# Performance work log

Measured on AMD Instinct MI355X. Metric: run time of the kernel, lower is better.

## Reference

```python
import jax, jax.numpy as jnp
import numpy as np

B, C, Hf, T = 8, 2, 257, 2048
D_IN = C * Hf          # 514
DM = 256               # d_model
NL = 4                 # n_layers
N = 32                 # S4D complex state size (d_state=64 -> N=32 complex modes)


def setup_inputs() -> dict:
    key = jax.random.key(0)
    ks = jax.random.split(key, 16)
    sc_in = 1.0 / np.sqrt(D_IN)
    sc_dm = 1.0 / np.sqrt(DM)
    inp = {}
    inp['x'] = jax.random.normal(ks[0], (B, C, Hf, T, 2), dtype=jnp.float32)
    # complex encoder (d_input -> d_model)
    inp['enc_Wr'] = jax.random.normal(ks[1], (DM, D_IN), dtype=jnp.float32) * sc_in
    inp['enc_Wi'] = jax.random.normal(ks[2], (DM, D_IN), dtype=jnp.float32) * sc_in
    inp['enc_br'] = jnp.zeros((DM,), jnp.float32)
    inp['enc_bi'] = jnp.zeros((DM,), jnp.float32)
    # per-layer S4D kernel params (stacked over layers)
    lo, hi = np.log(0.001), np.log(0.1)
    inp['log_dt'] = jax.random.uniform(ks[3], (NL, DM), dtype=jnp.float32) * (hi - lo) + lo
    inp['log_A_real'] = jnp.full((NL, DM, N), np.log(0.5), dtype=jnp.float32)
    inp['A_imag'] = jnp.broadcast_to(np.pi * jnp.arange(N, dtype=jnp.float32), (NL, DM, N)) + 0.0
    inp['C_r'] = jax.random.normal(ks[4], (NL, DM, N), dtype=jnp.float32)
    inp['C_i'] = jax.random.normal(ks[5], (NL, DM, N), dtype=jnp.float32)
    inp['D'] = jax.random.normal(ks[6], (NL, DM), dtype=jnp.float32)
    # per-layer complex pointwise output linear (d_model -> d_model)
    inp['out_Wr'] = jax.random.normal(ks[7], (NL, DM, DM), dtype=jnp.float32) * sc_dm
    inp['out_Wi'] = jax.random.normal(ks[8], (NL, DM, DM), dtype=jnp.float32) * sc_dm
    inp['out_br'] = jnp.zeros((NL, DM), jnp.float32)
    inp['out_bi'] = jnp.zeros((NL, DM), jnp.float32)
    # per-layer complex LayerNorm (separate real/imag affine)
    inp['ln_gamma_r'] = jnp.ones((NL, DM), jnp.float32)
    inp['ln_gamma_i'] = jnp.ones((NL, DM), jnp.float32)
    inp['ln_beta_r'] = jnp.zeros((NL, DM), jnp.float32)
    inp['ln_beta_i'] = jnp.zeros((NL, DM), jnp.float32)
    # complex decoder (d_model -> d_output = c*h)
    inp['dec_Wr'] = jax.random.normal(ks[9], (D_IN, DM), dtype=jnp.float32) * sc_dm
    inp['dec_Wi'] = jax.random.normal(ks[10], (D_IN, DM), dtype=jnp.float32) * sc_dm
    inp['dec_br'] = jnp.zeros((D_IN,), jnp.float32)
    inp['dec_bi'] = jnp.zeros((D_IN,), jnp.float32)
    return inp


def _clinear(xr, xi, Wr, Wi, br, bi):
    # complex linear: (xr + i xi) @ (Wr + i Wi)^T + (br + i bi)
    yr = xr @ Wr.T - xi @ Wi.T + br
    yi = xi @ Wr.T + xr @ Wi.T + bi
    return yr, yi


def _layernorm_ch(v, g, b, eps=1e-5):
    # normalize over channel axis 1 of (B, H, T)
    m = v.mean(axis=1, keepdims=True)
    var = ((v - m) ** 2).mean(axis=1, keepdims=True)
    return (v - m) / jnp.sqrt(var + eps) * g[None, :, None] + b[None, :, None]


def _forward(x, enc_Wr, enc_Wi, enc_br, enc_bi, log_dt, log_A_real, A_imag,
             C_r, C_i, D, out_Wr, out_Wi, out_br, out_bi,
             ln_gamma_r, ln_gamma_i, ln_beta_r, ln_beta_i,
             dec_Wr, dec_Wi, dec_br, dec_bi):
    b, c, h, T, _ = x.shape
    xf = x.reshape(b, c * h, T, 2)
    xf = jnp.swapaxes(xf, 1, 2)               # (b, T, c*h, 2)
    zr, zi = _clinear(xf[..., 0], xf[..., 1], enc_Wr, enc_Wi, enc_br, enc_bi)  # (b, T, DM)
    zr = jnp.swapaxes(zr, -1, -2)             # (b, DM, T)
    zi = jnp.swapaxes(zi, -1, -2)
    tgrid = jnp.arange(T, dtype=jnp.float32)
    n_layers = log_dt.shape[0]
    for l in range(n_layers):
        # ---- ComplexS4D kernel (diagonal SSM, ZOH-like discretization) ----
        dt = jnp.exp(log_dt[l])[:, None]                        # (H,1)
        A = -jnp.exp(log_A_real[l]) + 1j * A_imag[l]            # (H,N) complex
        dtA = A * dt                                            # (H,N)
        Ct = (C_r[l] + 1j * C_i[l]) * (jnp.exp(dtA) - 1.0) / A  # (H,N)
        K = jnp.einsum('hn,hnl->hl', Ct, jnp.exp(dtA[:, :, None] * tgrid))  # complex (H,T)
        # ---- complex FFT causal convolution ----
        u = zr + 1j * zi                                        # (b,H,T)
        y = jnp.fft.ifft(jnp.fft.fft(u, 2 * T) * jnp.fft.fft(K, 2 * T)[None])[..., :T]
        y = y + D[l][None, :, None] * u                         # skip connection
        yr = jax.nn.gelu(y.real)
        yi = jax.nn.gelu(y.imag)
        # ---- complex pointwise output linear ----
        orr = jnp.einsum('bht,gh->bgt', yr, out_Wr[l]) - jnp.einsum('bht,gh->bgt', yi, out_Wi[l]) + out_br[l][None, :, None]
        oii = jnp.einsum('bht,gh->bgt', yi, out_Wr[l]) + jnp.einsum('bht,gh->bgt', yr, out_Wi[l]) + out_bi[l][None, :, None]
        # residual + post-norm (prenorm=False), complex LayerNorm over d_model
        zr = _layernorm_ch(zr + orr, ln_gamma_r[l], ln_beta_r[l])
        zi = _layernorm_ch(zi + oii, ln_gamma_i[l], ln_beta_i[l])
    zr = jnp.swapaxes(zr, -1, -2)             # (b, T, DM)
    zi = jnp.swapaxes(zi, -1, -2)
    dr, di = _clinear(zr, zi, dec_Wr, dec_Wi, dec_br, dec_bi)  # (b, T, c*h)
    dr = jnp.swapaxes(dr, 1, 2)               # (b, c*h, T)
    di = jnp.swapaxes(di, 1, 2)
    return jnp.stack([dr, di], axis=-1).reshape(b, c, h, T, 2)


def reference(x, enc_Wr, enc_Wi, enc_br, enc_bi, log_dt, log_A_real, A_imag,
              C_r, C_i, D, out_Wr, out_Wi, out_br, out_bi,
              ln_gamma_r, ln_gamma_i, ln_beta_r, ln_beta_i,
              dec_Wr, dec_Wi, dec_br, dec_bi):
    return _forward(x, enc_Wr, enc_Wi, enc_br, enc_bi, log_dt, log_A_real, A_imag,
                    C_r, C_i, D, out_Wr, out_Wi, out_br, out_bi,
                    ln_gamma_r, ln_gamma_i, ln_beta_r, ln_beta_i,
                    dec_Wr, dec_Wi, dec_br, dec_bi)
```

## Files before the change

### kernel.cpp

```cpp
#include <hip/hip_runtime.h>
#include <cstddef>
#include <cstdint>


typedef __attribute__((ext_vector_type(8))) short short8;
typedef __attribute__((ext_vector_type(4))) float float4v;

__device__ __forceinline__ unsigned short f2bf(float f) {
    union { float f; unsigned u; } v; v.f = f;
    const unsigned r = v.u + 0x7fffu + ((v.u >> 16) & 1u);
    return (unsigned short)(r >> 16);
}

__device__ __forceinline__ float gelu_tanh(float x) {
    const float x3 = x * x * x;
    const float v  = 0.7978845608028654f * (x + 0.044715f * x3);
    const float e  = __expf(2.f * v);
    const float th = 1.f - 2.f / (e + 1.f);
    return 0.5f * x * (1.f + th);
}

__device__ __forceinline__ unsigned cvt_pk_bf16(float lo, float hi) {
    unsigned r;
    asm("v_cvt_pk_bf16_f32 %0, %1, %2" : "=v"(r) : "v"(lo), "v"(hi));
    return r;
}
__device__ __forceinline__ float2 unpk(unsigned d) {
    float2 u;
    u.x = __uint_as_float(d << 16);
    u.y = __uint_as_float(d & 0xffff0000u);
    return u;
}

__device__ __forceinline__ float2 cfma(const float2 w, const float2 p,
                                       const float2 u) {
    float2 t, r;
    asm("v_pk_fma_f32 %0, %1, %2, %3 op_sel:[1,1,0] op_sel_hi:[1,0,1] neg_lo:[1,0,0] neg_hi:[0,0,0]"
        : "=v"(t) : "v"(w), "v"(p), "v"(u));
    asm("v_pk_fma_f32 %0, %1, %2, %3 op_sel:[0,0,0] op_sel_hi:[0,1,1]"
        : "=v"(r) : "v"(w), "v"(p), "v"(t));
    return r;
}

template<int CTL>
__device__ __forceinline__ float dppadd(float x) {
    union { float f; int i; } a, r;
    a.f = x;
    r.i = __builtin_amdgcn_update_dpp(a.i, a.i, CTL, 0xF, 0xF, true);
    return x + r.f;
}
#define DPP_XOR1 0xB1
#define DPP_XOR2 0x4E

#define ASYNC_COPY16(gp, lp) __builtin_amdgcn_global_load_lds( \
    (const __attribute__((address_space(1))) unsigned int*)(gp), \
    (__attribute__((address_space(3))) unsigned int*)(lp), 16, 0, 0)

__global__ __launch_bounds__(256) void buildall_k(
    const float* __restrict__ enc_Wr, const float* __restrict__ enc_Wi,
    const float* __restrict__ out_Wr, const float* __restrict__ out_Wi,
    const float* __restrict__ dec_Wr, const float* __restrict__ dec_Wi,
    const float* __restrict__ enc_br, const float* __restrict__ enc_bi,
    const float* __restrict__ out_br, const float* __restrict__ out_bi,
    const float* __restrict__ dec_br, const float* __restrict__ dec_bi,
    unsigned short* __restrict__ A_enc, unsigned short* __restrict__ A_lay,
    unsigned short* __restrict__ A_dec,
    float* __restrict__ b_enc, float* __restrict__ b_lay,
    float* __restrict__ b_dec)
{
    int blk = blockIdx.x;
    const int tid = threadIdx.x;
    if (blk < 2112) {
        const int i = blk * 256 + tid;
        const int m = i / 1056, k = i - m * 1056;
        const int ri = m >= 256, g = m & 255;
        const int blk2 = k >= 528;
        const int hh = k - blk2 * 528;
        float val = 0.f;
        if (hh < 514) {
            const float wr = enc_Wr[(size_t)g * 514 + hh];
            const float wi = enc_Wi[(size_t)g * 514 + hh];
            val = ri ? (blk2 ? wr : wi) : (blk2 ? -wi : wr);
        }
        A_enc[i] = f2bf(val);
        return;
    }
    blk -= 2112;
    if (blk < 4096) {
        const int l = blk >> 10;
        const int i = ((blk & 1023) << 8) + tid;
        const float* Wr = out_Wr + (size_t)l * 65536;
        const float* Wi = out_Wi + (size_t)l * 65536;
        const int m = i >> 9, k = i & 511;
        const int ri = m >= 256, g = m & 255;
        const int blk2 = k >> 8, hh = k & 255;
        const float wr = Wr[(size_t)g * 256 + hh];
        const float wi = Wi[(size_t)g * 256 + hh];
        A_lay[(size_t)l * 262144 + i] =
            f2bf(ri ? (blk2 ? wr : wi) : (blk2 ? -wi : wr));
        return;
    }
    blk -= 4096;
    if (blk < 2304) {
        const int i = blk * 256 + tid;
        const int m = i >> 9, k = i & 511;
        const int g = m >> 1, comp = m & 1;
        float val = 0.f;
        if (g < 514) {
            const int blk2 = k >> 8, hh = k & 255;
            const float wr = dec_Wr[(size_t)g * 256 + hh];
            const float wi = dec_Wi[(size_t)g * 256 + hh];
            val = comp ? (blk2 ? wr : wi) : (blk2 ? -wi : wr);
        }
        A_dec[i] = f2bf(val);
        return;
    }
    blk -= 2304;
    if (blk < 2) {
        const int i = blk * 256 + tid;
        b_enc[i] = (i < 256) ? enc_br[i] : enc_bi[i - 256];
        return;
    }
    blk -= 2;
    if (blk < 8) {
        const int l = blk >> 1;
        const int i = ((blk & 1) << 8) + tid;
        b_lay[l * 512 + i] = (i < 256) ? out_br[l * 256 + i]
                                       : out_bi[l * 256 + i - 256];
        return;
    }
    blk -= 8;
    {
        const int i = blk * 256 + tid;
        if (i < 1028) b_dec[i] = (i & 1) ? dec_bi[i >> 1] : dec_br[i >> 1];
    }
}

__global__ __launch_bounds__(256) void packx_k(const float* __restrict__ x,
                                               unsigned short* __restrict__ xp)
{
    const int t0 = blockIdx.x * 64, d0 = blockIdx.y * 64, b = blockIdx.z;
    __shared__ unsigned short tr_[64][72];
    __shared__ unsigned short ti_[64][72];
    const int tid = threadIdx.x;
    const int tp = tid & 31, dl0 = tid >> 5;
#pragma unroll
    for (int p = 0; p < 8; ++p) {
        const int d = dl0 + p * 8;
        const int gd = d0 + d;
        float4 v = make_float4(0.f, 0.f, 0.f, 0.f);
        if (gd < 514) v = *(const float4*)(x + (((size_t)b * 514 + gd) * 2048 + t0 + tp * 2) * 2);
        tr_[tp * 2 + 0][d] = f2bf(v.x); ti_[tp * 2 + 0][d] = f2bf(v.y);
        tr_[tp * 2 + 1][d] = f2bf(v.z); ti_[tp * 2 + 1][d] = f2bf(v.w);
    }
    __syncthreads();
    const int dc = tid & 7;
    const int kloc = d0 + dc * 8;
    if (kloc < 528) {
#pragma unroll
        for (int p = 0; p < 2; ++p) {
            const int t = (tid >> 3) + p * 32;
            const size_t rowb = ((size_t)b * 2048 + t0 + t) * 1056;
            *(short8*)&xp[rowb + kloc]       = *(const short8*)&tr_[t][dc * 8];
            *(short8*)&xp[rowb + 528 + kloc] = *(const short8*)&ti_[t][dc * 8];
        }
    }
}

__global__ __launch_bounds__(256, 2) void mgemm_k(
    const unsigned short* __restrict__ A, const float* __restrict__ bias,
    const unsigned short* __restrict__ Bm, float* __restrict__ out,
    int M, int Kp)
{
    __shared__ unsigned short As[4096];
    __shared__ unsigned short Bs[4096];
    const int tid = threadIdx.x;
    const int w = tid >> 6, lane = tid & 63;
    const int m0 = blockIdx.x * 128, t0 = blockIdx.y * 128, b = blockIdx.z;
    const int wm = w & 1, wn = w >> 1;

    const unsigned short* Ab = A + (size_t)m0 * Kp;
    const unsigned short* Bb = Bm + ((size_t)b * 2048 + t0) * Kp;

    const int c0 = w * 64 + lane;
    const int r0 = c0 >> 2, q0 = (c0 & 3) * 8;
    const int c1 = c0 + 256;
    const int r1 = c1 >> 2, q1 = (c1 & 3) * 8;
    unsigned short* As0 = &As[(size_t)(w * 64) * 8];
    unsigned short* As1 = &As[(size_t)(w * 64 + 256) * 8];
    unsigned short* Bs0 = &Bs[(size_t)(w * 64) * 8];
    unsigned short* Bs1 = &Bs[(size_t)(w * 64 + 256) * 8];

    float4v acc[4][4];
#pragma unroll
    for (int i = 0; i < 4; ++i)
#pragma unroll
        for (int j = 0; j < 4; ++j) acc[i][j] = (float4v){0.f, 0.f, 0.f, 0.f};

    const int arow = wm * 64 + (lane & 15);
    const int brow = wn * 64 + (lane & 15);
    const int kq = (lane >> 4) * 8;

    for (int k0 = 0; k0 < Kp; k0 += 32) {
        ASYNC_COPY16(Ab + (size_t)r0 * Kp + k0 + q0, As0);
        ASYNC_COPY16(Ab + (size_t)r1 * Kp + k0 + q1, As1);
        ASYNC_COPY16(Bb + (size_t)r0 * Kp + k0 + q0, Bs0);
        ASYNC_COPY16(Bb + (size_t)r1 * Kp + k0 + q1, Bs1);
        __syncthreads();
        short8 af[4], bf[4];
#pragma unroll
        for (int i = 0; i < 4; ++i) af[i] = *(const short8*)&As[(arow + i * 16) * 32 + kq];
#pragma unroll
        for (int j = 0; j < 4; ++j) bf[j] = *(const short8*)&Bs[(brow + j * 16) * 32 + kq];
#pragma unroll
        for (int i = 0; i < 4; ++i)
#pragma unroll
            for (int j = 0; j < 4; ++j)
                acc[i][j] = __builtin_amdgcn_mfma_f32_16x16x32_bf16(af[i], bf[j], acc[i][j], 0, 0, 0);
        __syncthreads();
    }

    const int col = lane & 15;
    const int rq = (lane >> 4) * 4;
#pragma unroll
    for (int i = 0; i < 4; ++i) {
        const int mloc = wm * 64 + i * 16 + rq;
#pragma unroll
        for (int r = 0; r < 4; ++r) {
            const int m = m0 + mloc + r;
            const float bs = bias[m];
#pragma unroll
            for (int j = 0; j < 4; ++j) {
                const int t = t0 + wn * 64 + j * 16 + col;
                out[((size_t)b * 512 + m) * 2048 + t] = acc[i][j][r] + bs;
            }
        }
    }
}

__global__ __launch_bounds__(512, 2) void mgemmln_k(
    const unsigned short* __restrict__ A, const float* __restrict__ bias,
    const unsigned short* __restrict__ Bm, float* __restrict__ z,
    const float* __restrict__ gamr, const float* __restrict__ gami,
    const float* __restrict__ betr, const float* __restrict__ beti, int l)
{
    __shared__ unsigned short Bs[64][512];
    __shared__ float biasS[512], gamS[512], betS[512];
    __shared__ float sred[8][64][2];
    __shared__ float sstat[2][64][2];
    const int tid = threadIdx.x;
    const int w = tid >> 6, lane = tid & 63;
    const int t0g = blockIdx.x * 64, b = blockIdx.y;
    unsigned char* BsB = (unsigned char*)&Bs[0][0];

    {
        const unsigned short* ysrc = Bm + (size_t)b * 512 * 2048 + t0g;
        const int tseg = lane & 7;
        const int rloc = lane >> 3;
#pragma unroll
        for (int p = 0; p < 8; ++p) {
            const int krow = w * 8 + rloc + p * 64;
            const short8 v = *(const short8*)(ysrc + (size_t)krow * 2048 + tseg * 8);
#pragma unroll
            for (int j = 0; j < 8; ++j) {
                const int t = tseg * 8 + j;
                const int mask = (((t & 7) ^ ((t >> 3) & 7)) << 4);
                *(unsigned short*)(BsB + t * 1024 + ((krow * 2) ^ mask)) =
                    ((const unsigned short*)&v)[j];
            }
        }
        const int m = tid, g = m & 255, comp = m >> 8;
        biasS[m] = bias[m];
        gamS[m] = (comp ? gami : gamr)[l * 256 + g];
        betS[m] = (comp ? beti : betr)[l * 256 + g];
    }
    __syncthreads();

    float4v acc[4][4];
#pragma unroll
    for (int i = 0; i < 4; ++i)
#pragma unroll
        for (int j = 0; j < 4; ++j) acc[i][j] = (float4v){0.f, 0.f, 0.f, 0.f};

    const int brow = lane & 15;
    const int kq8 = (lane >> 4) * 8;
    const unsigned short* Ab = A + ((size_t)(w * 64 + brow)) * 512 + kq8;
    int baseB[4], maskB[4];
#pragma unroll
    for (int j = 0; j < 4; ++j) {
        const int t = j * 16 + brow;
        baseB[j] = t * 1024;
        maskB[j] = (((t & 7) ^ ((t >> 3) & 7)) << 4);
    }

#define LOADF(af_, bf_, k0_) do {                                              \
    _Pragma("unroll")                                                          \
    for (int i = 0; i < 4; ++i)                                                \
        af_[i] = *(const short8*)(Ab + (size_t)i * 16 * 512 + (k0_));          \
    _Pragma("unroll")                                                          \
    for (int j = 0; j < 4; ++j)                                                \
        bf_[j] = *(const short8*)(BsB + baseB[j] + ((((k0_) + kq8) * 2) ^ maskB[j])); \
} while (0)
#define MFMAS(af_, bf_) do {                                                   \
    _Pragma("unroll")                                                          \
    for (int i = 0; i < 4; ++i)                                                \
        _Pragma("unroll")                                                      \
        for (int j = 0; j < 4; ++j)                                            \
            acc[i][j] = __builtin_amdgcn_mfma_f32_16x16x32_bf16(af_[i], bf_[j], acc[i][j], 0, 0, 0); \
} while (0)

    {
        short8 afA[4], bfA[4], afB[4], bfB[4];
        LOADF(afA, bfA, 0);
#pragma unroll 1
        for (int kk = 0; kk < 16; kk += 2) {
            LOADF(afB, bfB, kk * 32 + 32);
            MFMAS(afA, bfA);
            if (kk + 2 < 16) LOADF(afA, bfA, kk * 32 + 64);
            MFMAS(afB, bfB);
        }
    }
#undef LOADF
#undef MFMAS

    const int q4 = (lane >> 4) * 4;
    float4 b4[4], g4[4], e4[4];
#pragma unroll
    for (int i = 0; i < 4; ++i) {
        const int m0 = w * 64 + i * 16 + q4;
        b4[i] = *(const float4*)&biasS[m0];
        g4[i] = *(const float4*)&gamS[m0];
        e4[i] = *(const float4*)&betS[m0];
    }

    float s1[4], s2[4];
#pragma unroll
    for (int j = 0; j < 4; ++j) { s1[j] = 0.f; s2[j] = 0.f; }
#pragma unroll
    for (int j = 0; j < 4; ++j) {
        const int t = t0g + j * 16 + brow;
#pragma unroll
        for (int i = 0; i < 4; ++i) {
            const int m = w * 64 + i * 16 + q4;
            const float* zp = &z[((size_t)b * 512 + m) * 2048 + t];
            const float bb[4] = {b4[i].x, b4[i].y, b4[i].z, b4[i].w};
#pragma unroll
            for (int r = 0; r < 4; ++r) {
                const float v = acc[i][j][r] + bb[r] + zp[(size_t)r * 2048];
                acc[i][j][r] = v;
                s1[j] += v; s2[j] += v * v;
            }
        }
    }
#pragma unroll
    for (int j = 0; j < 4; ++j) {
        s1[j] += __shfl_xor(s1[j], 16); s2[j] += __shfl_xor(s2[j], 16);
        s1[j] += __shfl_xor(s1[j], 32); s2[j] += __shfl_xor(s2[j], 32);
    }
    if (lane < 16) {
#pragma unroll
        for (int j = 0; j < 4; ++j) {
            sred[w][j * 16 + lane][0] = s1[j];
            sred[w][j * 16 + lane][1] = s2[j];
        }
    }
    __syncthreads();
    if (tid < 128) {
        const int t = tid & 63, comp = tid >> 6;
        float S1 = 0.f, S2 = 0.f;
#pragma unroll
        for (int w2 = 0; w2 < 4; ++w2) {
            S1 += sred[comp * 4 + w2][t][0];
            S2 += sred[comp * 4 + w2][t][1];
        }
        const float mn = S1 * (1.f / 256.f);
        const float var = S2 * (1.f / 256.f) - mn * mn;
        sstat[comp][t][0] = mn;
        sstat[comp][t][1] = rsqrtf(var + 1e-5f);
    }
    __syncthreads();
    const int comp = w >> 2;
#pragma unroll
    for (int j = 0; j < 4; ++j) {
        const int tl = j * 16 + brow;
        const float mn = sstat[comp][tl][0], rs = sstat[comp][tl][1];
        const int t = t0g + tl;
#pragma unroll
        for (int i = 0; i < 4; ++i) {
            const int m = w * 64 + i * 16 + q4;
            float* zp = &z[((size_t)b * 512 + m) * 2048 + t];
            const float gg[4] = {g4[i].x, g4[i].y, g4[i].z, g4[i].w};
            const float ee[4] = {e4[i].x, e4[i].y, e4[i].z, e4[i].w};
#pragma unroll
            for (int r = 0; r < 4; ++r)
                zp[(size_t)r * 2048] = (acc[i][j][r] - mn) * rs * gg[r] + ee[r];
        }
    }
}

__global__ __launch_bounds__(512, 2) void mgemmdec_k(
    const unsigned short* __restrict__ A, const float* __restrict__ bias,
    const float* __restrict__ z, float* __restrict__ out)
{
    __shared__ unsigned short Bs[64][512];
    const int tid = threadIdx.x;
    const int w = tid >> 6, lane = tid & 63;
    const int m0b = blockIdx.x * 384;
    const int t0g = blockIdx.y * 64, b = blockIdx.z;
    unsigned char* BsB = (unsigned char*)&Bs[0][0];

    {
        const float* zsrc = z + (size_t)b * 512 * 2048 + t0g;
        const int tseg = lane & 7, rloc = lane >> 3;
#pragma unroll
        for (int p = 0; p < 8; ++p) {
            const int krow = w * 8 + rloc + p * 64;
            const float* rowp = zsrc + (size_t)krow * 2048 + tseg * 8;
            const float4 va = *(const float4*)rowp;
            const float4 vb = *(const float4*)(rowp + 4);
            const float vals[8] = {va.x, va.y, va.z, va.w, vb.x, vb.y, vb.z, vb.w};
#pragma unroll
            for (int j = 0; j < 8; ++j) {
                const int t = tseg * 8 + j;
                const int mask = (((t & 7) ^ ((t >> 3) & 7)) << 4);
                *(unsigned short*)(BsB + t * 1024 + ((krow * 2) ^ mask)) = f2bf(vals[j]);
            }
        }
    }
    __syncthreads();

    float4v acc[3][4];
#pragma unroll
    for (int i = 0; i < 3; ++i)
#pragma unroll
        for (int j = 0; j < 4; ++j) acc[i][j] = (float4v){0.f, 0.f, 0.f, 0.f};

    const int brow = lane & 15;
    const int kq8 = (lane >> 4) * 8;
    const unsigned short* Ab = A + ((size_t)(m0b + w * 48 + brow)) * 512 + kq8;
    int baseB[4], maskB[4];
#pragma unroll
    for (int j = 0; j < 4; ++j) {
        const int t = j * 16 + brow;
        baseB[j] = t * 1024;
        maskB[j] = (((t & 7) ^ ((t >> 3) & 7)) << 4);
    }

#define LOADF(af_, bf_, k0_) do {                                              \
    _Pragma("unroll")                                                          \
    for (int i = 0; i < 3; ++i)                                                \
        af_[i] = *(const short8*)(Ab + (size_t)i * 16 * 512 + (k0_));          \
    _Pragma("unroll")                                                          \
    for (int j = 0; j < 4; ++j)                                                \
        bf_[j] = *(const short8*)(BsB + baseB[j] + ((((k0_) + kq8) * 2) ^ maskB[j])); \
} while (0)
#define MFMAS(af_, bf_) do {                                                   \
    _Pragma("unroll")                                                          \
    for (int i = 0; i < 3; ++i)                                                \
        _Pragma("unroll")                                                      \
        for (int j = 0; j < 4; ++j)                                            \
            acc[i][j] = __builtin_amdgcn_mfma_f32_16x16x32_bf16(af_[i], bf_[j], acc[i][j], 0, 0, 0); \
} while (0)

    {
        short8 afA[3], bfA[4], afB[3], bfB[4];
        LOADF(afA, bfA, 0);
#pragma unroll 1
        for (int kk = 0; kk < 16; kk += 2) {
            LOADF(afB, bfB, kk * 32 + 32);
            MFMAS(afA, bfA);
            if (kk + 2 < 16) LOADF(afA, bfA, kk * 32 + 64);
            MFMAS(afB, bfB);
        }
    }
#undef LOADF
#undef MFMAS

    const int q4 = (lane >> 4) * 4;
#pragma unroll
    for (int i = 0; i < 3; ++i) {
        const int mb = m0b + w * 48 + i * 16 + q4;
#pragma unroll
        for (int pr = 0; pr < 2; ++pr) {
            const int m2 = mb + pr * 2;
            const int g = m2 >> 1;
            if (g >= 514) continue;
            const float br = bias[m2], bi2 = bias[m2 + 1];
            float* op = out + (((size_t)b * 514 + g) * 2048 + t0g) * 2;
#pragma unroll
            for (int j = 0; j < 4; ++j) {
                const int tl = j * 16 + brow;
                const float2 v = make_float2(acc[i][j][pr * 2 + 0] + br,
                                             acc[i][j][pr * 2 + 1] + bi2);
                *(float2*)(op + (size_t)tl * 2) = v;
            }
        }
    }
}

__global__ __launch_bounds__(256, 6) void s4scan_k(
    const float* __restrict__ z, unsigned short* __restrict__ y,
    const float* __restrict__ log_dt, const float* __restrict__ log_A_real,
    const float* __restrict__ A_imag, const float* __restrict__ C_r,
    const float* __restrict__ C_i, const float* __restrict__ Dsk, int l)
{
    const int h = blockIdx.x, b = blockIdx.y;
    const int tid = threadIdx.x;
    const int lane = tid & 63, wv = tid >> 6;
    __shared__ float2 wsh[32], csh[32];
    __shared__ float dsh;
    __shared__ unsigned us[64][33];
    __shared__ __align__(16) unsigned char uni[64 * 33 * 8];
    float2 (*vsh2)[33] = (float2(*)[33])uni;
    float2 (*ys)[33]   = (float2(*)[33])uni;

    if (tid < 32) {
        const size_t pidx = ((size_t)l * 256 + h) * 32 + tid;
        const float dt = __expf(log_dt[l * 256 + h]);
        const float Ar = -__expf(log_A_real[pidx]);
        const float Ai = A_imag[pidx];
        const float er = __expf(Ar * dt);
        float sv, cv;
        __sincosf(Ai * dt, &sv, &cv);
        const float wr = er * cv, wi = er * sv;
        const float den = 1.f / (Ar * Ar + Ai * Ai);
        const float nr = wr - 1.f, ni = wi;
        const float qr = (nr * Ar + ni * Ai) * den;
        const float qi = (ni * Ar - nr * Ai) * den;
        const float cr = C_r[pidx], ci = C_i[pidx];
        wsh[tid] = make_float2(wr, wi);
        csh[tid] = make_float2(cr * qr - ci * qi, cr * qi + ci * qr);
    }
    if (tid == 32) dsh = Dsk[l * 256 + h];

    const int c0q = tid >> 2, t0q = (tid & 3) * 8;
    {
        const float* zrp = z + ((size_t)b * 512 + h) * 2048 + tid * 8;
        const float* zip = zrp + 256 * 2048;
        const float4 r0 = *(const float4*)zrp, r1 = *(const float4*)(zrp + 4);
        const float4 i0 = *(const float4*)zip, i1 = *(const float4*)(zip + 4);
        unsigned* up = &us[c0q][t0q];
        up[0] = cvt_pk_bf16(r0.x, i0.x); up[1] = cvt_pk_bf16(r0.y, i0.y);
        up[2] = cvt_pk_bf16(r0.z, i0.z); up[3] = cvt_pk_bf16(r0.w, i0.w);
        up[4] = cvt_pk_bf16(r1.x, i1.x); up[5] = cvt_pk_bf16(r1.y, i1.y);
        up[6] = cvt_pk_bf16(r1.z, i1.z); up[7] = cvt_pk_bf16(r1.w, i1.w);
    }
    __syncthreads();

    const float2 zero2 = make_float2(0.f, 0.f);

    {
        float2 w8[8], x8[8];
#pragma unroll
        for (int j = 0; j < 8; ++j) {
            w8[j] = wsh[wv * 8 + j];
            x8[j] = zero2;
        }
#pragma unroll 8
        for (int tt = 0; tt < 32; ++tt) {
            const float2 u = unpk(us[lane][tt]);
#pragma unroll
            for (int j = 0; j < 8; ++j) x8[j] = cfma(w8[j], x8[j], u);
        }
        const int dstc = (lane + 1) & 63;
#pragma unroll
        for (int j = 0; j < 8; ++j) {
            float2 f = w8[j];
#pragma unroll
            for (int s = 0; s < 5; ++s) f = cfma(f, f, zero2);
            float2 qv = x8[j], pq = f;
#pragma unroll
            for (int s = 0; s < 6; ++s) {
                const int d = 1 << s;
                float2 sh;
                sh.x = __shfl_up(qv.x, (unsigned)d);
                sh.y = __shfl_up(qv.y, (unsigned)d);
                const float2 qn = cfma(pq, sh, qv);
                if (lane >= d) qv = qn;
                pq = cfma(pq, pq, zero2);
            }
            vsh2[dstc][wv * 8 + j] = (lane == 63) ? zero2 : qv;
        }
    }
    __syncthreads();

    {
        const int q = tid & 3;
        float2 w8[8], c8[8], s8[8];
#pragma unroll
        for (int j = 0; j < 8; ++j) {
            const int n = q * 8 + j;
            w8[j] = wsh[n];
            c8[j] = csh[n];
            s8[j] = vsh2[c0q][n];
        }
        __syncthreads();
#pragma unroll 4
        for (int tt = 0; tt < 32; ++tt) {
            const float2 u = unpk(us[c0q][tt]);
            float2 py = zero2;
#pragma unroll
            for (int j = 0; j < 8; ++j) {
                s8[j] = cfma(w8[j], s8[j], u);
                py = cfma(c8[j], s8[j], py);
            }
            py.x = dppadd<DPP_XOR1>(py.x); py.x = dppadd<DPP_XOR2>(py.x);
            py.y = dppadd<DPP_XOR1>(py.y); py.y = dppadd<DPP_XOR2>(py.y);
            if (q == 0) ys[c0q][tt] = py;
        }
    }
    __syncthreads();

    {
        const float dv = dsh;
        unsigned short* yrp = y + ((size_t)b * 512 + h) * 2048 + tid * 8;
        unsigned short* yip = yrp + 256 * 2048;
        short8 vr8, vi8;
#pragma unroll
        for (int j = 0; j < 8; ++j) {
            const float2 yv = ys[c0q][t0q + j];
            const float2 uv = unpk(us[c0q][t0q + j]);
            ((unsigned short*)&vr8)[j] = f2bf(gelu_tanh(__builtin_fmaf(dv, uv.x, yv.x)));
            ((unsigned short*)&vi8)[j] = f2bf(gelu_tanh(__builtin_fmaf(dv, uv.y, yv.y)));
        }
        *(short8*)yrp = vr8;
        *(short8*)yip = vi8;
    }
}

extern "C" void kernel_launch(void* const* d_in, const int* in_sizes, int n_in,
                              void* d_out, int out_size, void* d_ws, size_t ws_size,
                              hipStream_t stream)
{
    const float* x        = (const float*)d_in[0];
    const float* enc_Wr   = (const float*)d_in[1];
    const float* enc_Wi   = (const float*)d_in[2];
    const float* enc_br   = (const float*)d_in[3];
    const float* enc_bi   = (const float*)d_in[4];
    const float* log_dt   = (const float*)d_in[5];
    const float* log_A_r  = (const float*)d_in[6];
    const float* A_imag   = (const float*)d_in[7];
    const float* C_r      = (const float*)d_in[8];
    const float* C_i      = (const float*)d_in[9];
    const float* Dp       = (const float*)d_in[10];
    const float* out_Wr   = (const float*)d_in[11];
    const float* out_Wi   = (const float*)d_in[12];
    const float* out_br   = (const float*)d_in[13];
    const float* out_bi   = (const float*)d_in[14];
    const float* ln_gr    = (const float*)d_in[15];
    const float* ln_gi    = (const float*)d_in[16];
    const float* ln_br    = (const float*)d_in[17];
    const float* ln_bi    = (const float*)d_in[18];
    const float* dec_Wr   = (const float*)d_in[19];
    const float* dec_Wi   = (const float*)d_in[20];
    const float* dec_br   = (const float*)d_in[21];
    const float* dec_bi   = (const float*)d_in[22];

    uint8_t* W = (uint8_t*)d_ws;
    float* z             = (float*)W;
    unsigned short* A_enc= (unsigned short*)(W + 50331648);
    unsigned short* A_lay= (unsigned short*)(W + 51412992);
    unsigned short* A_dec= (unsigned short*)(W + 53510144);
    float* b_enc         = (float*)(W + 54689792);
    float* b_lay         = (float*)(W + 54691840);
    float* b_dec         = (float*)(W + 54700032);

    unsigned short* y   = (unsigned short*)((uint8_t*)d_out + 33554432);
    unsigned short* xp  = (unsigned short*)d_out;

    buildall_k<<<8527, 256, 0, stream>>>(enc_Wr, enc_Wi, out_Wr, out_Wi,
                                         dec_Wr, dec_Wi, enc_br, enc_bi,
                                         out_br, out_bi, dec_br, dec_bi,
                                         A_enc, A_lay, A_dec,
                                         b_enc, b_lay, b_dec);

    packx_k<<<dim3(32, 9, 8), 256, 0, stream>>>(x, xp);
    mgemm_k<<<dim3(4, 16, 8), 256, 0, stream>>>(A_enc, b_enc, xp, z, 512, 1056);

    for (int l = 0; l < 4; ++l) {
        s4scan_k<<<dim3(256, 8), 256, 0, stream>>>(z, y, log_dt, log_A_r, A_imag, C_r, C_i, Dp, l);
        mgemmln_k<<<dim3(32, 8), 512, 0, stream>>>(A_lay + (size_t)l * 262144,
                                                   b_lay + l * 512, y, z,
                                                   ln_gr, ln_gi, ln_br, ln_bi, l);
    }

    mgemmdec_k<<<dim3(3, 32, 8), 512, 0, stream>>>(A_dec, b_dec, z, (float*)d_out);
}
```

Baseline: 570.6 us.

## Recast S4D chunked scan as MFMA matmuls with precomputed per-channel matrices

Replaces the scalar complex recurrences in the S4 scan (intra-chunk state accumulation and chunk output) with bf16 MFMA matrix products. The power matrix, Toeplitz kernel and state-to-output matrices are precomputed per channel by a new buildmm_k launch per layer. Inter-chunk state stays as the parallel prefix, and the carried state is split into hi/lo bf16 parts to keep precision. It trades scalar FMA work for matrix-core work but adds a kernel launch per layer, global matrix reads, and some bf16 rounding risk in the power and Toeplitz matrices.

Measured after the change: 530.8 us. 7.0% less time.

```diff
diff --git a/kernel.cpp b/kernel.cpp
--- a/kernel.cpp
+++ b/kernel.cpp
@@ -41,16 +41,6 @@
         : "=v"(r) : "v"(w), "v"(p), "v"(t));
     return r;
 }
-
-template<int CTL>
-__device__ __forceinline__ float dppadd(float x) {
-    union { float f; int i; } a, r;
-    a.f = x;
-    r.i = __builtin_amdgcn_update_dpp(a.i, a.i, CTL, 0xF, 0xF, true);
-    return x + r.f;
-}
-#define DPP_XOR1 0xB1
-#define DPP_XOR2 0x4E
 
 #define ASYNC_COPY16(gp, lp) __builtin_amdgcn_global_load_lds( \
     (const __attribute__((address_space(1))) unsigned int*)(gp), \
@@ -136,6 +126,72 @@
     }
 }
 
+__global__ __launch_bounds__(256) void buildmm_k(
+    const float* __restrict__ log_dt, const float* __restrict__ log_A_real,
+    const float* __restrict__ A_imag, const float* __restrict__ C_r,
+    const float* __restrict__ C_i, unsigned short* __restrict__ Pmat, int l)
+{
+    const int h = blockIdx.x;
+    const int tid = threadIdx.x;
+    __shared__ float2 pw[32][33];
+    __shared__ float2 csh[32], gsh[32];
+
+    if (tid < 32) {
+        const size_t pidx = ((size_t)l * 256 + h) * 32 + tid;
+        const float dt = __expf(log_dt[l * 256 + h]);
+        const float Ar = -__expf(log_A_real[pidx]);
+        const float Ai = A_imag[pidx];
+        const float er = __expf(Ar * dt);
+        float sv, cv;
+        __sincosf(Ai * dt, &sv, &cv);
+        const float wr = er * cv, wi = er * sv;
+        const float den = 1.f / (Ar * Ar + Ai * Ai);
+        const float nr = wr - 1.f, ni = wi;
+        const float qr = (nr * Ar + ni * Ai) * den;
+        const float qi = (ni * Ar - nr * Ai) * den;
+        const float cr = C_r[pidx], ci = C_i[pidx];
+        csh[tid] = make_float2(cr * qr - ci * qi, cr * qi + ci * qr);
+        float2 p = make_float2(1.f, 0.f);
+        const float2 w = make_float2(wr, wi);
+#pragma unroll 1
+        for (int k = 0; k < 33; ++k) {
+            pw[tid][k] = p;
+            const float pr = p.x * w.x - p.y * w.y;
+            p.y = p.x * w.y + p.y * w.x;
+            p.x = pr;
+        }
+    }
+    __syncthreads();
+    if (tid < 32) {
+        float2 g = make_float2(0.f, 0.f);
+#pragma unroll 1
+        for (int n = 0; n < 32; ++n) {
+            const float2 c = csh[n], p = pw[n][tid];
+            g.x += c.x * p.x - c.y * p.y;
+            g.y += c.x * p.y + c.y * p.x;
+        }
+        gsh[tid] = g;
+    }
+    __syncthreads();
+
+    unsigned short* base = Pmat + (size_t)h * 12288;
+    const int row = tid >> 2, cq = (tid & 3) * 16;
+    const int half = row & 1, src = row >> 1;
+#pragma unroll 1
+    for (int c = cq; c < cq + 16; ++c) {
+        const int ci = c & 1, idx = c >> 1;
+        const float2 v = pw[src][31 - idx];
+        base[row * 64 + c] = f2bf(half ? (ci ? v.x : v.y) : (ci ? -v.y : v.x));
+        const float2 g = (idx <= src) ? gsh[src - idx] : make_float2(0.f, 0.f);
+        base[4096 + row * 64 + c] = f2bf(half ? (ci ? g.x : g.y) : (ci ? -g.y : g.x));
+        const float2 wp = pw[idx][src + 1];
+        const float2 cc = csh[idx];
+        const float2 e = make_float2(cc.x * wp.x - cc.y * wp.y,
+                                     cc.x * wp.y + cc.y * wp.x);
+        base[8192 + row * 64 + c] = f2bf(half ? (ci ? e.x : e.y) : (ci ? -e.y : e.x));
+    }
+}
+
 __global__ __launch_bounds__(256) void packx_k(const float* __restrict__ x,
                                                unsigned short* __restrict__ xp)
 {
@@ -498,21 +554,21 @@
     }
 }
 
-__global__ __launch_bounds__(256, 6) void s4scan_k(
+__global__ __launch_bounds__(256) void s4mm_k(
     const float* __restrict__ z, unsigned short* __restrict__ y,
+    const unsigned short* __restrict__ Pmat,
     const float* __restrict__ log_dt, const float* __restrict__ log_A_real,
-    const float* __restrict__ A_imag, const float* __restrict__ C_r,
-    const float* __restrict__ C_i, const float* __restrict__ Dsk, int l)
+    const float* __restrict__ A_imag, const float* __restrict__ Dsk, int l)
 {
     const int h = blockIdx.x, b = blockIdx.y;
     const int tid = threadIdx.x;
     const int lane = tid & 63, wv = tid >> 6;
-    __shared__ float2 wsh[32], csh[32];
+    __shared__ float2 wsh[32];
     __shared__ float dsh;
-    __shared__ unsigned us[64][33];
-    __shared__ __align__(16) unsigned char uni[64 * 33 * 8];
-    float2 (*vsh2)[33] = (float2(*)[33])uni;
-    float2 (*ys)[33]   = (float2(*)[33])uni;
+    __shared__ unsigned Ub[64][36];
+    __shared__ unsigned Sb[64][36];
+    __shared__ unsigned Sc[64][36];
+    __shared__ float2 scr[64][33];
 
     if (tid < 32) {
         const size_t pidx = ((size_t)l * 256 + h) * 32 + tid;
@@ -522,53 +578,64 @@
         const float er = __expf(Ar * dt);
         float sv, cv;
         __sincosf(Ai * dt, &sv, &cv);
-        const float wr = er * cv, wi = er * sv;
-        const float den = 1.f / (Ar * Ar + Ai * Ai);
-        const float nr = wr - 1.f, ni = wi;
-        const float qr = (nr * Ar + ni * Ai) * den;
-        const float qi = (ni * Ar - nr * Ai) * den;
-        const float cr = C_r[pidx], ci = C_i[pidx];
-        wsh[tid] = make_float2(wr, wi);
-        csh[tid] = make_float2(cr * qr - ci * qi, cr * qi + ci * qr);
+        wsh[tid] = make_float2(er * cv, er * sv);
     }
     if (tid == 32) dsh = Dsk[l * 256 + h];
 
-    const int c0q = tid >> 2, t0q = (tid & 3) * 8;
+    const int c0q = tid >> 2, j0q = (tid & 3) * 8;
     {
         const float* zrp = z + ((size_t)b * 512 + h) * 2048 + tid * 8;
         const float* zip = zrp + 256 * 2048;
         const float4 r0 = *(const float4*)zrp, r1 = *(const float4*)(zrp + 4);
         const float4 i0 = *(const float4*)zip, i1 = *(const float4*)(zip + 4);
-        unsigned* up = &us[c0q][t0q];
-        up[0] = cvt_pk_bf16(r0.x, i0.x); up[1] = cvt_pk_bf16(r0.y, i0.y);
-        up[2] = cvt_pk_bf16(r0.z, i0.z); up[3] = cvt_pk_bf16(r0.w, i0.w);
-        up[4] = cvt_pk_bf16(r1.x, i1.x); up[5] = cvt_pk_bf16(r1.y, i1.y);
-        up[6] = cvt_pk_bf16(r1.z, i1.z); up[7] = cvt_pk_bf16(r1.w, i1.w);
-    }
-    __syncthreads();
-
+        uint4 pa, pb;
+        pa.x = cvt_pk_bf16(r0.x, i0.x); pa.y = cvt_pk_bf16(r0.y, i0.y);
+        pa.z = cvt_pk_bf16(r0.z, i0.z); pa.w = cvt_pk_bf16(r0.w, i0.w);
+        pb.x = cvt_pk_bf16(r1.x, i1.x); pb.y = cvt_pk_bf16(r1.y, i1.y);
+        pb.z = cvt_pk_bf16(r1.z, i1.z); pb.w = cvt_pk_bf16(r1.w, i1.w);
+        *(uint4*)&Ub[c0q][j0q]     = pa;
+        *(uint4*)&Ub[c0q][j0q + 4] = pb;
+    }
+    __syncthreads();
+
+    const unsigned short* Pg = Pmat + (size_t)h * 12288;
+    const int bcol = lane & 15, kq = (lane >> 4) * 8;
+    const int arow = (wv * 16 + bcol) * 64 + kq;
     const float2 zero2 = make_float2(0.f, 0.f);
 
     {
-        float2 w8[8], x8[8];
-#pragma unroll
-        for (int j = 0; j < 8; ++j) {
-            w8[j] = wsh[wv * 8 + j];
-            x8[j] = zero2;
-        }
-#pragma unroll 8
-        for (int tt = 0; tt < 32; ++tt) {
-            const float2 u = unpk(us[lane][tt]);
-#pragma unroll
-            for (int j = 0; j < 8; ++j) x8[j] = cfma(w8[j], x8[j], u);
-        }
+        float4v a1[4];
+#pragma unroll
+        for (int jf = 0; jf < 4; ++jf) a1[jf] = (float4v){0.f, 0.f, 0.f, 0.f};
+#pragma unroll
+        for (int k0 = 0; k0 < 64; k0 += 32) {
+            const short8 af = *(const short8*)(Pg + arow + k0);
+#pragma unroll
+            for (int jf = 0; jf < 4; ++jf) {
+                const short8 bf = *(const short8*)&Ub[16 * jf + bcol][(k0 + kq) >> 1];
+                a1[jf] = __builtin_amdgcn_mfma_f32_16x16x32_bf16(af, bf, a1[jf], 0, 0, 0);
+            }
+        }
+        const int mode0 = (wv * 16 + (lane >> 4) * 4) >> 1;
+#pragma unroll
+        for (int jf = 0; jf < 4; ++jf) {
+            const int c = 16 * jf + bcol;
+            scr[c][mode0]     = make_float2(a1[jf][0], a1[jf][1]);
+            scr[c][mode0 + 1] = make_float2(a1[jf][2], a1[jf][3]);
+        }
+    }
+    __syncthreads();
+
+    {
         const int dstc = (lane + 1) & 63;
-#pragma unroll
-        for (int j = 0; j < 8; ++j) {
-            float2 f = w8[j];
+#pragma unroll 1
+        for (int jm = 0; jm < 8; ++jm) {
+            const int n = wv * 8 + jm;
+            const float2 wm = wsh[n];
+            float2 f = wm;
 #pragma unroll
             for (int s = 0; s < 5; ++s) f = cfma(f, f, zero2);
-            float2 qv = x8[j], pq = f;
+            float2 qv = scr[lane][n], pq = f;
 #pragma unroll
             for (int s = 0; s < 6; ++s) {
                 const int d = 1 << s;
@@ -579,34 +646,55 @@
                 if (lane >= d) qv = qn;
                 pq = cfma(pq, pq, zero2);
             }
-            vsh2[dstc][wv * 8 + j] = (lane == 63) ? zero2 : qv;
-        }
-    }
-    __syncthreads();
-
-    {
-        const int q = tid & 3;
-        float2 w8[8], c8[8], s8[8];
-#pragma unroll
-        for (int j = 0; j < 8; ++j) {
-            const int n = q * 8 + j;
-            w8[j] = wsh[n];
-            c8[j] = csh[n];
-            s8[j] = vsh2[c0q][n];
+            const unsigned hi = cvt_pk_bf16(qv.x, qv.y);
+            const float2 hv = unpk(hi);
+            const unsigned lo = cvt_pk_bf16(qv.x - hv.x, qv.y - hv.y);
+            Sb[dstc][n] = (lane == 63) ? 0u : hi;
+            Sc[dstc][n] = (lane == 63) ? 0u : lo;
+        }
+    }
+    __syncthreads();
+
+    {
+        const unsigned short* Tg = Pg + 4096;
+        const unsigned short* Mg = Pg + 8192;
+        float4v a2[4];
+#pragma unroll
+        for (int jf = 0; jf < 4; ++jf) a2[jf] = (float4v){0.f, 0.f, 0.f, 0.f};
+#pragma unroll
+        for (int k0 = 0; k0 < 64; k0 += 32) {
+            const short8 af = *(const short8*)(Tg + arow + k0);
+#pragma unroll
+            for (int jf = 0; jf < 4; ++jf) {
+                const short8 bf = *(const short8*)&Ub[16 * jf + bcol][(k0 + kq) >> 1];
+                a2[jf] = __builtin_amdgcn_mfma_f32_16x16x32_bf16(af, bf, a2[jf], 0, 0, 0);
+            }
+        }
+#pragma unroll
+        for (int k0 = 0; k0 < 64; k0 += 32) {
+            const short8 af = *(const short8*)(Mg + arow + k0);
+#pragma unroll
+            for (int jf = 0; jf < 4; ++jf) {
+                const short8 bf = *(const short8*)&Sb[16 * jf + bcol][(k0 + kq) >> 1];
+                a2[jf] = __builtin_amdgcn_mfma_f32_16x16x32_bf16(af, bf, a2[jf], 0, 0, 0);
+            }
+        }
+#pragma unroll
+        for (int k0 = 0; k0 < 64; k0 += 32) {
+            const short8 af = *(const short8*)(Mg + arow + k0);
+#pragma unroll
+            for (int jf = 0; jf < 4; ++jf) {
+                const short8 bf = *(const short8*)&Sc[16 * jf + bcol][(k0 + kq) >> 1];
+                a2[jf] = __builtin_amdgcn_mfma_f32_16x16x32_bf16(af, bf, a2[jf], 0, 0, 0);
+            }
         }
         __syncthreads();
-#pragma unroll 4
-        for (int tt = 0; tt < 32; ++tt) {
-            const float2 u = unpk(us[c0q][tt]);
-            float2 py = zero2;
-#pragma unroll
-            for (int j = 0; j < 8; ++j) {
-                s8[j] = cfma(w8[j], s8[j], u);
-                py = cfma(c8[j], s8[j], py);
-            }
-            py.x = dppadd<DPP_XOR1>(py.x); py.x = dppadd<DPP_XOR2>(py.x);
-            py.y = dppadd<DPP_XOR1>(py.y); py.y = dppadd<DPP_XOR2>(py.y);
-            if (q == 0) ys[c0q][tt] = py;
+        const int jp0 = (wv * 16 + (lane >> 4) * 4) >> 1;
+#pragma unroll
+        for (int jf = 0; jf < 4; ++jf) {
+            const int c = 16 * jf + bcol;
+            scr[c][jp0]     = make_float2(a2[jf][0], a2[jf][1]);
+            scr[c][jp0 + 1] = make_float2(a2[jf][2], a2[jf][3]);
         }
     }
     __syncthreads();
@@ -618,8 +706,8 @@
         short8 vr8, vi8;
 #pragma unroll
         for (int j = 0; j < 8; ++j) {
-            const float2 yv = ys[c0q][t0q + j];
-            const float2 uv = unpk(us[c0q][t0q + j]);
+            const float2 yv = scr[c0q][j0q + j];
+            const float2 uv = unpk(Ub[c0q][j0q + j]);
             ((unsigned short*)&vr8)[j] = f2bf(gelu_tanh(__builtin_fmaf(dv, uv.x, yv.x)));
             ((unsigned short*)&vi8)[j] = f2bf(gelu_tanh(__builtin_fmaf(dv, uv.y, yv.y)));
         }
@@ -658,6 +746,7 @@
 
     uint8_t* W = (uint8_t*)d_ws;
     float* z             = (float*)W;
+    unsigned short* Pmat = (unsigned short*)(W + 33554432);
     unsigned short* A_enc= (unsigned short*)(W + 50331648);
     unsigned short* A_lay= (unsigned short*)(W + 51412992);
     unsigned short* A_dec= (unsigned short*)(W + 53510144);
@@ -678,7 +767,9 @@
     mgemm_k<<<dim3(4, 16, 8), 256, 0, stream>>>(A_enc, b_enc, xp, z, 512, 1056);
 
     for (int l = 0; l < 4; ++l) {
-        s4scan_k<<<dim3(256, 8), 256, 0, stream>>>(z, y, log_dt, log_A_r, A_imag, C_r, C_i, Dp, l);
+        buildmm_k<<<256, 256, 0, stream>>>(log_dt, log_A_r, A_imag, C_r, C_i, Pmat, l);
+        s4mm_k<<<dim3(256, 8), 256, 0, stream>>>(z, y, Pmat, log_dt, log_A_r,
+                                                 A_imag, Dp, l);
         mgemmln_k<<<dim3(32, 8), 512, 0, stream>>>(A_lay + (size_t)l * 262144,
                                                    b_lay + l * 512, y, z,
                                                    ln_gr, ln_gi, ln_br, ln_bi, l);
```
